# Kernel tuning notes

Measured on AMD Instinct MI355X. Metric: run time of the kernel, lower is better.

Reference implementation:

```python
import jax, jax.numpy as jnp
import numpy as np

DIM = 1024
NUM_HEADS = 16
DIM_HEAD = 64
INNER = NUM_HEADS * DIM_HEAD  # 1024
SCALE = DIM_HEAD ** -0.5


def setup_inputs() -> dict:
    key = jax.random.key(0)
    ks = jax.random.split(key, 8)
    B, SQ, SK = 2, 2048, 4096
    x = jax.random.normal(ks[0], (B, SQ, DIM), dtype=jnp.float32)
    context = jax.random.normal(ks[1], (B, SK, DIM), dtype=jnp.float32)
    # LayerNorm params
    ln_gamma = jnp.ones((DIM,), jnp.float32)
    ln_beta = jnp.zeros((DIM,), jnp.float32)
    # Linear weights, stored as [in, out] so y = x @ W (torch Linear weight transposed)
    w_q = jax.random.normal(ks[2], (DIM, INNER), dtype=jnp.float32) / np.sqrt(DIM)
    w_kv = jax.random.normal(ks[3], (DIM, 2 * INNER), dtype=jnp.float32) / np.sqrt(DIM)
    w_out = jax.random.normal(ks[4], (INNER, DIM), dtype=jnp.float32) / np.sqrt(INNER)
    b_out = jnp.zeros((DIM,), jnp.float32)
    # torch init is 0.0 (tanh(0)=0); use a nonzero value so output/grads are nontrivial
    gate = jnp.array([0.5], jnp.float32)
    return {"x": x, "context": context, "ln_gamma": ln_gamma, "ln_beta": ln_beta,
            "w_q": w_q, "w_kv": w_kv, "w_out": w_out, "b_out": b_out, "gate": gate}


def _layernorm(x, gamma, beta, eps=1e-5):
    mu = jnp.mean(x, axis=-1, keepdims=True)
    var = jnp.mean(jnp.square(x - mu), axis=-1, keepdims=True)
    return (x - mu) * jax.lax.rsqrt(var + eps) * gamma + beta


def reference(x, context, ln_gamma, ln_beta, w_q, w_kv, w_out, b_out, gate):
    B, SQ, _ = x.shape
    SK = context.shape[1]
    xn = _layernorm(x, ln_gamma, ln_beta)
    q = (xn @ w_q).reshape(B, SQ, NUM_HEADS, DIM_HEAD)
    kv = context @ w_kv
    k, v = jnp.split(kv, 2, axis=-1)
    k = k.reshape(B, SK, NUM_HEADS, DIM_HEAD)
    v = v.reshape(B, SK, NUM_HEADS, DIM_HEAD)
    # scores: [B, H, SQ, SK]
    scores = jnp.einsum('bqhd,bkhd->bhqk', q * SCALE, k)
    attn = jax.nn.softmax(scores, axis=-1)
    out = jnp.einsum('bhqk,bkhd->bqhd', attn, v).reshape(B, SQ, INNER)
    out = out @ w_out + b_out
    return out * jnp.tanh(gate[0])
```

## Files before the change

### kernel.cpp

```cpp
#include <hip/hip_runtime.h>
#include <hip/hip_bf16.h>
#include <stdint.h>

#define DIMM  1024
#define NHEAD 16
#define DHEAD 64
#define BB    2
#define SQL   2048
#define SKL   4096
#define KVW   2048
#define NT    (SKL / 64)

typedef __attribute__((ext_vector_type(8))) short short8;
typedef __attribute__((ext_vector_type(4))) float f32x4;
typedef __attribute__((ext_vector_type(16))) float f32x16;
typedef __attribute__((ext_vector_type(4))) unsigned short us4;

typedef const __attribute__((address_space(1))) uint32_t gu32_t;
typedef __attribute__((address_space(3))) uint32_t lu32_t;

#define GLDS16(gp, lp) __builtin_amdgcn_global_load_lds((gu32_t*)(gp), (lu32_t*)(lp), 16, 0, 0)

static __device__ __forceinline__ unsigned short f2bf(float f) {
  union { float f; uint32_t u; } v; v.f = f;
  uint32_t r = v.u + 0x7fffu + ((v.u >> 16) & 1u);
  return (unsigned short)(r >> 16);
}

__global__ __launch_bounds__(256) void k_transpose_cast(const float* __restrict__ in,
                                                        unsigned short* __restrict__ out,
                                                        int K, int N) {
  __shared__ float tile[32][33];
  int n0 = blockIdx.x * 32, k0 = blockIdx.y * 32;
  int tx = threadIdx.x, ty = threadIdx.y;
  #pragma unroll
  for (int i = 0; i < 4; i++)
    tile[ty + i * 8][tx] = in[(size_t)(k0 + ty + i * 8) * N + n0 + tx];
  __syncthreads();
  #pragma unroll
  for (int i = 0; i < 4; i++)
    out[(size_t)(n0 + ty + i * 8) * K + k0 + tx] = f2bf(tile[tx][ty + i * 8]);
}

__global__ __launch_bounds__(256) void k_cast(const float* __restrict__ in,
                                              unsigned short* __restrict__ out) {
  size_t i = (size_t)(blockIdx.x * 256 + threadIdx.x) * 4;
  float4 v = *(const float4*)(in + i);
  us4 o;
  o.x = f2bf(v.x); o.y = f2bf(v.y); o.z = f2bf(v.z); o.w = f2bf(v.w);
  *(us4*)(out + i) = o;
}

__global__ __launch_bounds__(256) void k_ln(const float* __restrict__ x,
                                            const float* __restrict__ gamma,
                                            const float* __restrict__ beta,
                                            unsigned short* __restrict__ out) {
  const int row = blockIdx.x, tid = threadIdx.x;
  const float* xr = x + (size_t)row * DIMM;
  float4 v = *(const float4*)(xr + tid * 4);
  float s = v.x + v.y + v.z + v.w;
  float ss = v.x * v.x + v.y * v.y + v.z * v.z + v.w * v.w;
  #pragma unroll
  for (int m = 1; m < 64; m <<= 1) {
    s += __shfl_xor(s, m);
    ss += __shfl_xor(ss, m);
  }
  __shared__ float red[8];
  const int wid = tid >> 6, lane = tid & 63;
  if (lane == 0) { red[wid] = s; red[4 + wid] = ss; }
  __syncthreads();
  s = red[0] + red[1] + red[2] + red[3];
  ss = red[4] + red[5] + red[6] + red[7];
  float mu = s * (1.0f / DIMM);
  float var = ss * (1.0f / DIMM) - mu * mu;
  float rstd = rsqrtf(var + 1e-5f);
  float4 g = *(const float4*)(gamma + tid * 4);
  float4 bt = *(const float4*)(beta + tid * 4);
  us4 o;
  o.x = f2bf((v.x - mu) * rstd * g.x + bt.x);
  o.y = f2bf((v.y - mu) * rstd * g.y + bt.y);
  o.z = f2bf((v.z - mu) * rstd * g.z + bt.z);
  o.w = f2bf((v.w - mu) * rstd * g.w + bt.w);
  *(us4*)(out + (size_t)row * DIMM + tid * 4) = o;
}

template<int MODE>
__global__ __launch_bounds__(256) void k_gemm_bt(const unsigned short* __restrict__ A,
                                                 const unsigned short* __restrict__ BT,
                                                 void* __restrict__ Cv,
                                                 int M, int N, int K,
                                                 const float* __restrict__ bias,
                                                 const float* __restrict__ gate) {
  __shared__ unsigned short lA[2][128 * 32];
  __shared__ unsigned short lB[2][128 * 32];
  const int tid = threadIdx.x;
  const int wid = tid >> 6, lane = tid & 63;
  const int kg = lane >> 4, lr = lane & 15;
  const int wr = wid >> 1, wc = wid & 1;
  const int im = blockIdx.x, in_ = blockIdx.y;
  const int nt = K >> 5;
  const size_t baseA = (size_t)im * 128 * K;
  const size_t baseB = (size_t)in_ * 128 * K;

  f32x4 acc[4][4];
  #pragma unroll
  for (int m = 0; m < 4; m++)
    #pragma unroll
    for (int n = 0; n < 4; n++) {
      f32x4 z = {0.0f, 0.0f, 0.0f, 0.0f};
      acc[m][n] = z;
    }

  auto GSTAGE = [&](int bufi, int t) {
    int k0 = t << 5;
    #pragma unroll
    for (int j = 0; j < 2; j++) {
      int e = wid * 1024 + j * 512 + lane * 8;
      int row = e >> 5;
      int g = (e >> 3) & 3;
      int col = (g ^ ((row >> 1) & 3)) << 3;
      GLDS16(A + baseA + (size_t)row * K + k0 + col, &lA[bufi][e]);
      GLDS16(BT + baseB + (size_t)row * K + k0 + col, &lB[bufi][e]);
    }
  };

  GSTAGE(0, 0);
  __syncthreads();
  int buf = 0;
  for (int t = 0; t < nt; t++) {
    if (t + 1 < nt) GSTAGE(buf ^ 1, t + 1);
    short8 a[4], b[4];
    #pragma unroll
    for (int m = 0; m < 4; m++) {
      int row = wr * 64 + m * 16 + lr;
      a[m] = *(const short8*)&lA[buf][row * 32 + ((kg ^ ((row >> 1) & 3)) << 3)];
    }
    #pragma unroll
    for (int n = 0; n < 4; n++) {
      int row = wc * 64 + n * 16 + lr;
      b[n] = *(const short8*)&lB[buf][row * 32 + ((kg ^ ((row >> 1) & 3)) << 3)];
    }
    #pragma unroll
    for (int m = 0; m < 4; m++)
      #pragma unroll
      for (int n = 0; n < 4; n++)
        acc[m][n] = __builtin_amdgcn_mfma_f32_16x16x32_bf16(a[m], b[n], acc[m][n], 0, 0, 0);
    __syncthreads();
    buf ^= 1;
  }

  const int r0 = im * 128 + wr * 64;
  const int c0 = in_ * 128 + wc * 64;
  if constexpr (MODE == 0) {
    unsigned short* C = (unsigned short*)Cv;
    #pragma unroll
    for (int m = 0; m < 4; m++)
      #pragma unroll
      for (int n = 0; n < 4; n++)
        #pragma unroll
        for (int j = 0; j < 4; j++)
          C[(size_t)(r0 + m * 16 + kg * 4 + j) * N + c0 + n * 16 + lr] = f2bf(acc[m][n][j]);
  } else {
    float* C = (float*)Cv;
    float gl = tanhf(gate[0]);
    #pragma unroll
    for (int m = 0; m < 4; m++)
      #pragma unroll
      for (int n = 0; n < 4; n++)
        #pragma unroll
        for (int j = 0; j < 4; j++) {
          int col = c0 + n * 16 + lr;
          C[(size_t)(r0 + m * 16 + kg * 4 + j) * N + col] = (acc[m][n][j] + bias[col]) * gl;
        }
  }
}

__global__ __launch_bounds__(256, 4) void k_attn(const unsigned short* __restrict__ Q,
                                                 const unsigned short* __restrict__ KV,
                                                 unsigned short* __restrict__ O) {
  __shared__ unsigned short sK[2][64 * 64];
  __shared__ unsigned short sV[2][64 * 64];

  const int tid = threadIdx.x;
  const int wave = tid >> 6, lane = tid & 63;
  const int wq = wave & 1, wk = wave >> 1;
  const int l31 = lane & 31, hi = lane >> 5;

  const int wid_b = blockIdx.x;
  const int work = (wid_b & 7) * 128 + (wid_b >> 3);
  const int qb = work & 31, bh = work >> 5;
  const int b = bh >> 4, h = bh & 15;

  const unsigned short* Qp = Q + (size_t)b * SQL * DIMM + h * DHEAD;
  const unsigned short* Kp = KV + (size_t)b * SKL * KVW + h * DHEAD;
  const unsigned short* Vp = Kp + DIMM;

  const int qr0 = qb * 64 + wq * 32;

  const unsigned short* ksrc[2]; int kdst[2];
  const unsigned short* vsrc[2]; int vdst[2];
  #pragma unroll
  for (int j = 0; j < 2; j++) {
    int e = (tid + j * 256) * 8;
    int row = e >> 6;
    int col = (((e >> 3) & 7) ^ (row & 7)) << 3;
    ksrc[j] = Kp + (size_t)row * KVW + col;
    kdst[j] = e;
    int g = tid + j * 256;
    int key = (g >> 5) * 4 + ((g >> 1) & 3);
    int d0v = ((g >> 3) & 3) * 16 + (g & 1) * 8;
    vsrc[j] = Vp + (size_t)key * KVW + d0v;
    vdst[j] = g * 8;
  }

  auto STAGE = [&](int bufi, int kt) {
    size_t off = (size_t)kt * 64 * KVW;
    #pragma unroll
    for (int j = 0; j < 2; j++) GLDS16(ksrc[j] + off, &sK[bufi][kdst[j]]);
    #pragma unroll
    for (int j = 0; j < 2; j++) GLDS16(vsrc[j] + off, &sV[bufi][vdst[j]]);
  };

  short8 qa[4];
  #pragma unroll
  for (int t = 0; t < 4; t++) {
    short8 v = *(const short8*)(Qp + (size_t)(qr0 + l31) * DIMM + t * 16 + hi * 8);
    #pragma unroll
    for (int j = 0; j < 8; j++) {
      union { float f; uint32_t u; } c;
      c.u = ((uint32_t)(unsigned short)v[j]) << 16;
      v[j] = (short)f2bf(c.f * 0.1803368801111f);
    }
    qa[t] = v;
  }

  f32x16 oacc[2];
  #pragma unroll
  for (int d2 = 0; d2 < 2; d2++)
    #pragma unroll
    for (int r = 0; r < 16; r++) oacc[d2][r] = 0.0f;
  float rs = 0.0f;

  const uint32_t sVb0 = (uint32_t)(size_t)(lu32_t*)&sV[0][0] +
                        (uint32_t)(hi * 1024 + ((lane >> 4) & 1) * 128 + (lane & 15) * 8);

  STAGE(0, 0);
  __syncthreads();

  union u4s8 { uint32_t u[4]; short8 s; };

  int buf = 0;
  for (int kt = 0; kt < NT; kt++) {
    if (kt + 1 < NT) STAGE(buf ^ 1, kt + 1);

    short8 kbf[4];
    {
      int row = wk * 32 + l31;
      #pragma unroll
      for (int t = 0; t < 4; t++) {
        int gl = t * 2 + hi;
        kbf[t] = *(const short8*)&sK[buf][row * 64 + ((gl ^ (row & 7)) << 3)];
      }
    }

    f32x16 sc;
    #pragma unroll
    for (int r = 0; r < 16; r++) sc[r] = 0.0f;
    #pragma unroll
    for (int t = 0; t < 4; t++)
      sc = __builtin_amdgcn_mfma_f32_32x32x16_bf16(kbf[t], qa[t], sc, 0, 0, 0);

    float p[16];
    #pragma unroll
    for (int r = 0; r < 16; r++) {
      p[r] = __builtin_amdgcn_exp2f(sc[r]);
      rs += p[r];
    }
    uint32_t w[8];
    #pragma unroll
    for (int i = 0; i < 8; i++)
      asm("v_cvt_pk_bf16_f32 %0, %1, %2" : "=v"(w[i]) : "v"(p[2 * i]), "v"(p[2 * i + 1]));
    asm("v_permlane32_swap_b32 %0, %1" : "+v"(w[0]), "+v"(w[2]));
    asm("v_permlane32_swap_b32 %0, %1" : "+v"(w[1]), "+v"(w[3]));
    asm("v_permlane32_swap_b32 %0, %1" : "+v"(w[4]), "+v"(w[6]));
    asm("v_permlane32_swap_b32 %0, %1" : "+v"(w[5]), "+v"(w[7]));
    u4s8 paf[2];
    paf[0].u[0] = w[0]; paf[0].u[1] = w[1]; paf[0].u[2] = w[2]; paf[0].u[3] = w[3];
    paf[1].u[0] = w[4]; paf[1].u[1] = w[5]; paf[1].u[2] = w[6]; paf[1].u[3] = w[7];

    u4s8 vb[2][2];
    {
      uint32_t tb = sVb0 + (uint32_t)(buf * 8192 + wk * 4096);
      #pragma unroll
      for (int d2 = 0; d2 < 2; d2++)
        #pragma unroll
        for (int ks = 0; ks < 2; ks++) {
          uint2 t0, t1;
          uint32_t a0 = tb + (uint32_t)(ks * 2048 + d2 * 256);
          asm volatile("ds_read_b64_tr_b16 %0, %1" : "=v"(t0) : "v"(a0));
          asm volatile("ds_read_b64_tr_b16 %0, %1" : "=v"(t1) : "v"(a0 + 512u));
          vb[d2][ks].u[0] = t0.x; vb[d2][ks].u[1] = t0.y;
          vb[d2][ks].u[2] = t1.x; vb[d2][ks].u[3] = t1.y;
        }
    }
    asm volatile("s_waitcnt lgkmcnt(0)" ::: "memory");
    __builtin_amdgcn_sched_barrier(0);

    #pragma unroll
    for (int d2 = 0; d2 < 2; d2++)
      #pragma unroll
      for (int ks = 0; ks < 2; ks++)
        oacc[d2] = __builtin_amdgcn_mfma_f32_32x32x16_bf16(paf[ks].s, vb[d2][ks].s, oacc[d2], 0, 0, 0);

    __syncthreads();
    buf ^= 1;
  }

  float* sRed = (float*)&sK[0][0];
  float* sRs  = (float*)&sV[0][0];
  if (wk == 1) {
    #pragma unroll
    for (int d2 = 0; d2 < 2; d2++)
      #pragma unroll
      for (int r = 0; r < 16; r++)
        sRed[((wq * 2 + d2) * 16 + r) * 64 + lane] = oacc[d2][r];
    sRs[wq * 64 + lane] = rs;
  }
  __syncthreads();
  if (wk == 0) {
    #pragma unroll
    for (int d2 = 0; d2 < 2; d2++)
      #pragma unroll
      for (int r = 0; r < 16; r++)
        oacc[d2][r] += sRed[((wq * 2 + d2) * 16 + r) * 64 + lane];
    float rs2 = rs + sRs[wq * 64 + lane];
    float t = rs2 + __shfl_xor(rs2, 32);
    float inv = 1.0f / t;
    float rq[16];
    #pragma unroll
    for (int r = 0; r < 16; r++) {
      int rho = (r & 3) + 8 * (r >> 2) + 4 * hi;
      rq[r] = __shfl(inv, rho);
    }
    unsigned short* Op = O + (size_t)b * SQL * DIMM + h * DHEAD;
    #pragma unroll
    for (int d2 = 0; d2 < 2; d2++)
      #pragma unroll
      for (int r = 0; r < 16; r++) {
        int rho = (r & 3) + 8 * (r >> 2) + 4 * hi;
        Op[(size_t)(qr0 + rho) * DIMM + d2 * 32 + l31] = f2bf(oacc[d2][r] * rq[r]);
      }
  }
}

extern "C" void kernel_launch(void* const* d_in, const int* in_sizes, int n_in,
                              void* d_out, int out_size, void* d_ws, size_t ws_size,
                              hipStream_t stream) {
  (void)in_sizes; (void)n_in; (void)out_size; (void)ws_size;
  const float* x     = (const float*)d_in[0];
  const float* ctx   = (const float*)d_in[1];
  const float* gamma = (const float*)d_in[2];
  const float* beta  = (const float*)d_in[3];
  const float* w_q   = (const float*)d_in[4];
  const float* w_kv  = (const float*)d_in[5];
  const float* w_out = (const float*)d_in[6];
  const float* b_out = (const float*)d_in[7];
  const float* gate  = (const float*)d_in[8];
  float* out = (float*)d_out;
  char* ws = (char*)d_ws;

  unsigned short* XN   = (unsigned short*)(ws);
  unsigned short* QB   = (unsigned short*)(ws + (8ull  << 20));
  unsigned short* CTXB = (unsigned short*)(ws + (16ull << 20));
  unsigned short* KVB  = (unsigned short*)(ws + (32ull << 20));
  unsigned short* OB   = (unsigned short*)(ws + (64ull << 20));
  unsigned short* WQT  = (unsigned short*)(ws + (72ull << 20));
  unsigned short* WKVT = (unsigned short*)(ws + (74ull << 20));
  unsigned short* WOT  = (unsigned short*)(ws + (78ull << 20));

  k_transpose_cast<<<dim3(32, 32), dim3(32, 8), 0, stream>>>(w_q, WQT, 1024, 1024);
  k_transpose_cast<<<dim3(64, 32), dim3(32, 8), 0, stream>>>(w_kv, WKVT, 1024, 2048);
  k_transpose_cast<<<dim3(32, 32), dim3(32, 8), 0, stream>>>(w_out, WOT, 1024, 1024);
  k_cast<<<dim3(8192), dim3(256), 0, stream>>>(ctx, CTXB);
  k_ln<<<dim3(4096), dim3(256), 0, stream>>>(x, gamma, beta, XN);
  k_gemm_bt<0><<<dim3(32, 8), dim3(256), 0, stream>>>(XN, WQT, QB, 4096, 1024, 1024, nullptr, nullptr);
  k_gemm_bt<0><<<dim3(64, 16), dim3(256), 0, stream>>>(CTXB, WKVT, KVB, 8192, 2048, 1024, nullptr, nullptr);
  k_attn<<<dim3(1024), dim3(256), 0, stream>>>(QB, KVB, OB);
  k_gemm_bt<1><<<dim3(32, 8), dim3(256), 0, stream>>>(OB, WOT, out, 4096, 1024, 1024, b_out, gate);
}
```

Before: 221.4 us.

## Fuse context cast into KV GEMM, merge Q/KV projections, retile output GEMM

Drops the standalone context fp32→bf16 cast kernel. The KV projection now loads fp32 context through registers, converts it with packed bf16 conversion and writes it into LDS. The Q and KV projections are merged into one launch with a grid-swizzled work mapping, which fills the GPU better. The output projection uses 64-row tiles, giving 512 blocks instead of 256, and the attention MFMA sections get raised wave priority. The risk is that the register-staged fp32 A path exposes global load latency and adds VGPR pressure.

```diff
diff --git a/kernel.cpp b/kernel.cpp
--- a/kernel.cpp
+++ b/kernel.cpp
@@ -40,15 +40,6 @@
   #pragma unroll
   for (int i = 0; i < 4; i++)
     out[(size_t)(n0 + ty + i * 8) * K + k0 + tx] = f2bf(tile[tx][ty + i * 8]);
-}
-
-__global__ __launch_bounds__(256) void k_cast(const float* __restrict__ in,
-                                              unsigned short* __restrict__ out) {
-  size_t i = (size_t)(blockIdx.x * 256 + threadIdx.x) * 4;
-  float4 v = *(const float4*)(in + i);
-  us4 o;
-  o.x = f2bf(v.x); o.y = f2bf(v.y); o.z = f2bf(v.z); o.w = f2bf(v.w);
-  *(us4*)(out + i) = o;
 }
 
 __global__ __launch_bounds__(256) void k_ln(const float* __restrict__ x,
@@ -84,23 +75,48 @@
   *(us4*)(out + (size_t)row * DIMM + tid * 4) = o;
 }
 
-template<int MODE>
-__global__ __launch_bounds__(256) void k_gemm_bt(const unsigned short* __restrict__ A,
-                                                 const unsigned short* __restrict__ BT,
-                                                 void* __restrict__ Cv,
-                                                 int M, int N, int K,
-                                                 const float* __restrict__ bias,
-                                                 const float* __restrict__ gate) {
+__global__ __launch_bounds__(256) void k_proj(const float* __restrict__ ctx,
+                                              const unsigned short* __restrict__ XN,
+                                              const unsigned short* __restrict__ WKVT,
+                                              const unsigned short* __restrict__ WQT,
+                                              unsigned short* __restrict__ KVB,
+                                              unsigned short* __restrict__ QB) {
   __shared__ unsigned short lA[2][128 * 32];
   __shared__ unsigned short lB[2][128 * 32];
   const int tid = threadIdx.x;
   const int wid = tid >> 6, lane = tid & 63;
   const int kg = lane >> 4, lr = lane & 15;
   const int wr = wid >> 1, wc = wid & 1;
-  const int im = blockIdx.x, in_ = blockIdx.y;
-  const int nt = K >> 5;
-  const size_t baseA = (size_t)im * 128 * K;
+  const int K = 1024, nt = 32;
+
+  const int bid = blockIdx.x;
+  const int w = (bid & 7) * 160 + (bid >> 3);
+  const bool isQ = (w >= 1024);
+  int im, in_, N;
+  const unsigned short* Bw;
+  unsigned short* Cout;
+  if (isQ) { int w2 = w - 1024; im = w2 & 31; in_ = w2 >> 5; Bw = WQT;  Cout = QB;  N = 1024; }
+  else     {                    im = w  & 63; in_ = w  >> 6; Bw = WKVT; Cout = KVB; N = 2048; }
   const size_t baseB = (size_t)in_ * 128 * K;
+  const unsigned short* Abf = XN + (size_t)im * 128 * K;
+  const float* Af = ctx + (size_t)im * 128 * K;
+
+  int ed[2], grow[2], gcol[2];
+  #pragma unroll
+  for (int j = 0; j < 2; j++) {
+    int e = wid * 1024 + j * 512 + lane * 8;
+    ed[j] = e;
+    int row = e >> 5;
+    grow[j] = row;
+    gcol[j] = (((e >> 3) & 3) ^ ((row >> 1) & 3)) << 3;
+  }
+  uint32_t awoff[4];
+  #pragma unroll
+  for (int p = 0; p < 4; p++) {
+    int row = p * 32 + (tid >> 3);
+    int g = (tid & 7) >> 1;
+    awoff[p] = (uint32_t)(row * 64 + ((g ^ ((row >> 1) & 3)) << 4) + (tid & 1) * 8);
+  }
 
   f32x4 acc[4][4];
   #pragma unroll
@@ -111,28 +127,148 @@
       acc[m][n] = z;
     }
 
-  auto GSTAGE = [&](int bufi, int t) {
+  float4 va[4];
+  auto STAGE_B = [&](int bufi, int t) {
     int k0 = t << 5;
     #pragma unroll
-    for (int j = 0; j < 2; j++) {
-      int e = wid * 1024 + j * 512 + lane * 8;
-      int row = e >> 5;
-      int g = (e >> 3) & 3;
-      int col = (g ^ ((row >> 1) & 3)) << 3;
-      GLDS16(A + baseA + (size_t)row * K + k0 + col, &lA[bufi][e]);
-      GLDS16(BT + baseB + (size_t)row * K + k0 + col, &lB[bufi][e]);
-    }
-  };
-
-  GSTAGE(0, 0);
+    for (int j = 0; j < 2; j++)
+      GLDS16(Bw + baseB + (size_t)grow[j] * K + k0 + gcol[j], &lB[bufi][ed[j]]);
+  };
+  auto STAGE_A_Q = [&](int bufi, int t) {
+    int k0 = t << 5;
+    #pragma unroll
+    for (int j = 0; j < 2; j++)
+      GLDS16(Abf + (size_t)grow[j] * K + k0 + gcol[j], &lA[bufi][ed[j]]);
+  };
+  auto LOAD_A_F32 = [&](int t) {
+    int k0 = t << 5;
+    #pragma unroll
+    for (int p = 0; p < 4; p++)
+      va[p] = *(const float4*)(Af + (size_t)(p * 32 + (tid >> 3)) * K + k0 + (tid & 7) * 4);
+  };
+  auto WRITE_A_F32 = [&](int bufi) {
+    #pragma unroll
+    for (int p = 0; p < 4; p++) {
+      uint32_t lo, hi;
+      asm("v_cvt_pk_bf16_f32 %0, %1, %2" : "=v"(lo) : "v"(va[p].x), "v"(va[p].y));
+      asm("v_cvt_pk_bf16_f32 %0, %1, %2" : "=v"(hi) : "v"(va[p].z), "v"(va[p].w));
+      uint2 w2; w2.x = lo; w2.y = hi;
+      *(uint2*)((char*)&lA[bufi][0] + awoff[p]) = w2;
+    }
+  };
+  auto COMPUTE = [&](int bufi) {
+    short8 a[4], b[4];
+    #pragma unroll
+    for (int m = 0; m < 4; m++) {
+      int row = wr * 64 + m * 16 + lr;
+      a[m] = *(const short8*)&lA[bufi][row * 32 + ((kg ^ ((row >> 1) & 3)) << 3)];
+    }
+    #pragma unroll
+    for (int n = 0; n < 4; n++) {
+      int row = wc * 64 + n * 16 + lr;
+      b[n] = *(const short8*)&lB[bufi][row * 32 + ((kg ^ ((row >> 1) & 3)) << 3)];
+    }
+    #pragma unroll
+    for (int m = 0; m < 4; m++)
+      #pragma unroll
+      for (int n = 0; n < 4; n++)
+        acc[m][n] = __builtin_amdgcn_mfma_f32_16x16x32_bf16(a[m], b[n], acc[m][n], 0, 0, 0);
+  };
+
+  int buf = 0;
+  if (isQ) {
+    STAGE_A_Q(0, 0); STAGE_B(0, 0);
+    __syncthreads();
+    for (int t = 0; t < nt; t++) {
+      if (t + 1 < nt) { STAGE_A_Q(buf ^ 1, t + 1); STAGE_B(buf ^ 1, t + 1); }
+      COMPUTE(buf);
+      __syncthreads();
+      buf ^= 1;
+    }
+  } else {
+    LOAD_A_F32(0); STAGE_B(0, 0); WRITE_A_F32(0);
+    __syncthreads();
+    for (int t = 0; t < nt; t++) {
+      if (t + 1 < nt) { LOAD_A_F32(t + 1); STAGE_B(buf ^ 1, t + 1); }
+      COMPUTE(buf);
+      if (t + 1 < nt) WRITE_A_F32(buf ^ 1);
+      __syncthreads();
+      buf ^= 1;
+    }
+  }
+
+  const int r0 = im * 128 + wr * 64;
+  const int c0 = in_ * 128 + wc * 64;
+  #pragma unroll
+  for (int m = 0; m < 4; m++)
+    #pragma unroll
+    for (int n = 0; n < 4; n++)
+      #pragma unroll
+      for (int j = 0; j < 4; j++)
+        Cout[(size_t)(r0 + m * 16 + kg * 4 + j) * N + c0 + n * 16 + lr] = f2bf(acc[m][n][j]);
+}
+
+__global__ __launch_bounds__(256) void k_out(const unsigned short* __restrict__ A,
+                                             const unsigned short* __restrict__ BT,
+                                             float* __restrict__ C,
+                                             const float* __restrict__ bias,
+                                             const float* __restrict__ gate) {
+  __shared__ unsigned short lA[2][64 * 32];
+  __shared__ unsigned short lB[2][128 * 32];
+  const int tid = threadIdx.x;
+  const int wid = tid >> 6, lane = tid & 63;
+  const int kg = lane >> 4, lr = lane & 15;
+  const int wr = wid >> 1, wc = wid & 1;
+  const int K = 1024, nt = 32, N = 1024;
+
+  const int bid = blockIdx.x;
+  const int w = (bid & 7) * 64 + (bid >> 3);
+  const int im = w & 63, in_ = w >> 6;
+  const size_t baseA = (size_t)im * 64 * K;
+  const size_t baseB = (size_t)in_ * 128 * K;
+
+  int eA, arow, acol;
+  {
+    int e = tid * 8;
+    eA = e;
+    int row = e >> 5;
+    arow = row; acol = (((e >> 3) & 3) ^ ((row >> 1) & 3)) << 3;
+  }
+  int eB[2], brow[2], bcol[2];
+  #pragma unroll
+  for (int j = 0; j < 2; j++) {
+    int e = tid * 8 + j * 2048;
+    eB[j] = e;
+    int row = e >> 5;
+    brow[j] = row; bcol[j] = (((e >> 3) & 3) ^ ((row >> 1) & 3)) << 3;
+  }
+
+  f32x4 acc[2][4];
+  #pragma unroll
+  for (int m = 0; m < 2; m++)
+    #pragma unroll
+    for (int n = 0; n < 4; n++) {
+      f32x4 z = {0.0f, 0.0f, 0.0f, 0.0f};
+      acc[m][n] = z;
+    }
+
+  auto STAGE = [&](int bufi, int t) {
+    int k0 = t << 5;
+    GLDS16(A + baseA + (size_t)arow * K + k0 + acol, &lA[bufi][eA]);
+    #pragma unroll
+    for (int j = 0; j < 2; j++)
+      GLDS16(BT + baseB + (size_t)brow[j] * K + k0 + bcol[j], &lB[bufi][eB[j]]);
+  };
+
+  STAGE(0, 0);
   __syncthreads();
   int buf = 0;
   for (int t = 0; t < nt; t++) {
-    if (t + 1 < nt) GSTAGE(buf ^ 1, t + 1);
-    short8 a[4], b[4];
-    #pragma unroll
-    for (int m = 0; m < 4; m++) {
-      int row = wr * 64 + m * 16 + lr;
+    if (t + 1 < nt) STAGE(buf ^ 1, t + 1);
+    short8 a[2], b[4];
+    #pragma unroll
+    for (int m = 0; m < 2; m++) {
+      int row = wr * 32 + m * 16 + lr;
       a[m] = *(const short8*)&lA[buf][row * 32 + ((kg ^ ((row >> 1) & 3)) << 3)];
     }
     #pragma unroll
@@ -141,7 +277,7 @@
       b[n] = *(const short8*)&lB[buf][row * 32 + ((kg ^ ((row >> 1) & 3)) << 3)];
     }
     #pragma unroll
-    for (int m = 0; m < 4; m++)
+    for (int m = 0; m < 2; m++)
       #pragma unroll
       for (int n = 0; n < 4; n++)
         acc[m][n] = __builtin_amdgcn_mfma_f32_16x16x32_bf16(a[m], b[n], acc[m][n], 0, 0, 0);
@@ -149,30 +285,18 @@
     buf ^= 1;
   }
 
-  const int r0 = im * 128 + wr * 64;
+  const int r0 = im * 64 + wr * 32;
   const int c0 = in_ * 128 + wc * 64;
-  if constexpr (MODE == 0) {
-    unsigned short* C = (unsigned short*)Cv;
-    #pragma unroll
-    for (int m = 0; m < 4; m++)
-      #pragma unroll
-      for (int n = 0; n < 4; n++)
-        #pragma unroll
-        for (int j = 0; j < 4; j++)
-          C[(size_t)(r0 + m * 16 + kg * 4 + j) * N + c0 + n * 16 + lr] = f2bf(acc[m][n][j]);
-  } else {
-    float* C = (float*)Cv;
-    float gl = tanhf(gate[0]);
-    #pragma unroll
-    for (int m = 0; m < 4; m++)
-      #pragma unroll
-      for (int n = 0; n < 4; n++)
-        #pragma unroll
-        for (int j = 0; j < 4; j++) {
-          int col = c0 + n * 16 + lr;
-          C[(size_t)(r0 + m * 16 + kg * 4 + j) * N + col] = (acc[m][n][j] + bias[col]) * gl;
-        }
-  }
+  float gl = tanhf(gate[0]);
+  #pragma unroll
+  for (int m = 0; m < 2; m++)
+    #pragma unroll
+    for (int n = 0; n < 4; n++)
+      #pragma unroll
+      for (int j = 0; j < 4; j++) {
+        int col = c0 + n * 16 + lr;
+        C[(size_t)(r0 + m * 16 + kg * 4 + j) * N + col] = (acc[m][n][j] + bias[col]) * gl;
+      }
 }
 
 __global__ __launch_bounds__(256, 4) void k_attn(const unsigned short* __restrict__ Q,
@@ -266,9 +390,11 @@
     f32x16 sc;
     #pragma unroll
     for (int r = 0; r < 16; r++) sc[r] = 0.0f;
+    __builtin_amdgcn_s_setprio(1);
     #pragma unroll
     for (int t = 0; t < 4; t++)
       sc = __builtin_amdgcn_mfma_f32_32x32x16_bf16(kbf[t], qa[t], sc, 0, 0, 0);
+    __builtin_amdgcn_s_setprio(0);
 
     float p[16];
     #pragma unroll
@@ -306,11 +432,13 @@
     asm volatile("s_waitcnt lgkmcnt(0)" ::: "memory");
     __builtin_amdgcn_sched_barrier(0);
 
+    __builtin_amdgcn_s_setprio(1);
     #pragma unroll
     for (int d2 = 0; d2 < 2; d2++)
       #pragma unroll
       for (int ks = 0; ks < 2; ks++)
         oacc[d2] = __builtin_amdgcn_mfma_f32_32x32x16_bf16(paf[ks].s, vb[d2][ks].s, oacc[d2], 0, 0, 0);
+    __builtin_amdgcn_s_setprio(0);
 
     __syncthreads();
     buf ^= 1;
@@ -371,7 +499,6 @@
 
   unsigned short* XN   = (unsigned short*)(ws);
   unsigned short* QB   = (unsigned short*)(ws + (8ull  << 20));
-  unsigned short* CTXB = (unsigned short*)(ws + (16ull << 20));
   unsigned short* KVB  = (unsigned short*)(ws + (32ull << 20));
   unsigned short* OB   = (unsigned short*)(ws + (64ull << 20));
   unsigned short* WQT  = (unsigned short*)(ws + (72ull << 20));
@@ -381,10 +508,8 @@
   k_transpose_cast<<<dim3(32, 32), dim3(32, 8), 0, stream>>>(w_q, WQT, 1024, 1024);
   k_transpose_cast<<<dim3(64, 32), dim3(32, 8), 0, stream>>>(w_kv, WKVT, 1024, 2048);
   k_transpose_cast<<<dim3(32, 32), dim3(32, 8), 0, stream>>>(w_out, WOT, 1024, 1024);
-  k_cast<<<dim3(8192), dim3(256), 0, stream>>>(ctx, CTXB);
   k_ln<<<dim3(4096), dim3(256), 0, stream>>>(x, gamma, beta, XN);
-  k_gemm_bt<0><<<dim3(32, 8), dim3(256), 0, stream>>>(XN, WQT, QB, 4096, 1024, 1024, nullptr, nullptr);
-  k_gemm_bt<0><<<dim3(64, 16), dim3(256), 0, stream>>>(CTXB, WKVT, KVB, 8192, 2048, 1024, nullptr, nullptr);
+  k_proj<<<dim3(1280), dim3(256), 0, stream>>>(ctx, XN, WKVT, WQT, KVB, QB);
   k_attn<<<dim3(1024), dim3(256), 0, stream>>>(QB, KVB, OB);
-  k_gemm_bt<1><<<dim3(32, 8), dim3(256), 0, stream>>>(OB, WOT, out, 4096, 1024, 1024, b_out, gate);
-}
+  k_out<<<dim3(512), dim3(256), 0, stream>>>(OB, WOT, out, b_out, gate);
+}
```

New measurement: 237.9 us. +7.5%, slower.
